# Kernel tuning notes

Hardware: AMD Instinct MI355X
Metric: run time of the kernel (lower is better)

## Reference

```python
import jax, jax.numpy as jnp
import numpy as np

N = 100000
E = 6400000
D = 512


def setup_inputs() -> dict:
    key = jax.random.key(0)
    k1, k2, k3, k4 = jax.random.split(key, 4)
    x = jax.random.normal(k1, (N, D), dtype=jnp.float32)
    edge_index = jax.random.randint(k2, (2, E), 0, N, dtype=jnp.int64)
    edge_attr = jax.random.uniform(k3, (E,), dtype=jnp.float32)
    # xavier_normal_ on (in_feat, 1) with gain=1.414: std = gain*sqrt(2/(fan_in+fan_out))
    std = 1.414 * np.sqrt(2.0 / (D + 1))
    p = jax.random.normal(k4, (D, 1), dtype=jnp.float32) * std
    b = jnp.zeros((1,), dtype=jnp.float32)
    return {"x": x, "edge_index": edge_index, "edge_attr": edge_attr, "p": p, "b": b}


def reference(x, edge_index, edge_attr, p, b):
    # Per-node gate: sigmoid(x @ p + b), shape [N]
    diag_val = jax.nn.sigmoid(jnp.matmul(x, p) + b).reshape(-1)
    # spspmm(A, diag(d)) scales each edge value by d[col] = d[edge_index[1]]
    adj_mat_val = edge_attr * diag_val[edge_index[1]]
    return edge_index, adj_mat_val
```

## Files before the change

kernel.cpp:

```cpp
#include <hip/hip_runtime.h>
#include <math.h>


__global__ __launch_bounds__(256) void gate_kernel(
    const float* __restrict__ x,
    const float* __restrict__ p,
    const float* __restrict__ b,
    float* __restrict__ gate,
    int N)
{
    const int wave_id = (blockIdx.x * blockDim.x + threadIdx.x) >> 6;
    const int lane    = threadIdx.x & 63;
    const int nwaves  = (gridDim.x * blockDim.x) >> 6;
    const float bb = b[0];

    const float4* pr = (const float4*)p;
    float4 p0 = pr[lane * 2];
    float4 p1 = pr[lane * 2 + 1];

    for (int row = wave_id; row < N; row += nwaves) {
        const float4* xr = (const float4*)(x + (size_t)row * 512);
        float4 x0 = xr[lane * 2];
        float4 x1 = xr[lane * 2 + 1];
        float s = x0.x * p0.x + x0.y * p0.y + x0.z * p0.z + x0.w * p0.w
                + x1.x * p1.x + x1.y * p1.y + x1.z * p1.z + x1.w * p1.w;
        #pragma unroll
        for (int off = 32; off > 0; off >>= 1)
            s += __shfl_down(s, off, 64);
        if (lane == 0) {
            float t = s + bb;
            gate[row] = 1.0f / (1.0f + __expf(-t));
        }
    }
}

__global__ __launch_bounds__(256) void edge_kernel(
    const int*   __restrict__ edge_index,
    const float* __restrict__ edge_attr,
    const float* __restrict__ gate,
    float* __restrict__ out,
    int E)
{
    const int tid    = blockIdx.x * blockDim.x + threadIdx.x;
    const int stride = gridDim.x * blockDim.x;

    const int EI4 = (2 * E) >> 2;
    const int EV4 = E >> 2;

    const int4*  ei4  = (const int4*)edge_index;
    float4*      out4 = (float4*)out;
    for (int i = tid; i < EI4; i += stride) {
        int4 v = ei4[i];
        out4[i] = make_float4((float)v.x, (float)v.y, (float)v.z, (float)v.w);
    }

    const int4*   col4 = (const int4*)(edge_index + E);
    const float4* ea4  = (const float4*)edge_attr;
    float4*       ov4  = (float4*)(out + 2 * (size_t)E);
    for (int i = tid; i < EV4; i += stride) {
        int4   c = col4[i];
        float4 a = ea4[i];
        float4 r;
        r.x = a.x * gate[c.x];
        r.y = a.y * gate[c.y];
        r.z = a.z * gate[c.z];
        r.w = a.w * gate[c.w];
        ov4[i] = r;
    }
}

extern "C" void kernel_launch(void* const* d_in, const int* in_sizes, int n_in,
                              void* d_out, int out_size, void* d_ws, size_t ws_size,
                              hipStream_t stream) {
    const float* x          = (const float*)d_in[0];
    const int*   edge_index = (const int*)  d_in[1];
    const float* edge_attr  = (const float*)d_in[2];
    const float* p          = (const float*)d_in[3];
    const float* b          = (const float*)d_in[4];

    const int D = in_sizes[3];
    const int N = in_sizes[0] / D;
    const int E = in_sizes[2];

    float* gate = (float*)d_ws;
    float* out  = (float*)d_out;

    int gate_blocks = (N + 3) / 4;
    gate_kernel<<<gate_blocks, 256, 0, stream>>>(x, p, b, gate, N);

    int edge_blocks = ((2 * E / 4) + 255) / 256;
    edge_kernel<<<edge_blocks, 256, 0, stream>>>(edge_index, edge_attr, gate, out, E);
}
```

Baseline: 370.2 us.

## Process two rows per wave in gate kernel and fuse edge index copy into value loop

The gate kernel now has each wave compute two rows, with a strided lane layout where lane i reads float4 i and i+64, so consecutive lanes load contiguous addresses. This gives more loads in flight per wave and uses half the waves. The edge kernel merges the index-to-float conversion loop into the value loop, so each thread reads row, col and attr once and writes all three outputs. This removes a second pass and reuses the already loaded column indices. The edge grid is halved to match.

```diff
diff --git a/kernel.cpp b/kernel.cpp
--- a/kernel.cpp
+++ b/kernel.cpp
@@ -11,25 +11,40 @@
 {
     const int wave_id = (blockIdx.x * blockDim.x + threadIdx.x) >> 6;
     const int lane    = threadIdx.x & 63;
-    const int nwaves  = (gridDim.x * blockDim.x) >> 6;
     const float bb = b[0];
 
     const float4* pr = (const float4*)p;
-    float4 p0 = pr[lane * 2];
-    float4 p1 = pr[lane * 2 + 1];
+    const float4 p0 = pr[lane];
+    const float4 p1 = pr[lane + 64];
 
-    for (int row = wave_id; row < N; row += nwaves) {
-        const float4* xr = (const float4*)(x + (size_t)row * 512);
-        float4 x0 = xr[lane * 2];
-        float4 x1 = xr[lane * 2 + 1];
-        float s = x0.x * p0.x + x0.y * p0.y + x0.z * p0.z + x0.w * p0.w
-                + x1.x * p1.x + x1.y * p1.y + x1.z * p1.z + x1.w * p1.w;
-        #pragma unroll
-        for (int off = 32; off > 0; off >>= 1)
-            s += __shfl_down(s, off, 64);
-        if (lane == 0) {
-            float t = s + bb;
-            gate[row] = 1.0f / (1.0f + __expf(-t));
+    const int row0 = wave_id * 2;
+    if (row0 >= N) return;
+    const bool two = (row0 + 1) < N;
+
+    const float4* xr0 = (const float4*)(x + (size_t)row0 * 512);
+    const float4* xr1 = (const float4*)(x + (size_t)(two ? row0 + 1 : row0) * 512);
+
+    float4 a0 = xr0[lane];
+    float4 a1 = xr0[lane + 64];
+    float4 c0 = xr1[lane];
+    float4 c1 = xr1[lane + 64];
+
+    float s0 = a0.x * p0.x + a0.y * p0.y + a0.z * p0.z + a0.w * p0.w
+             + a1.x * p1.x + a1.y * p1.y + a1.z * p1.z + a1.w * p1.w;
+    float s1 = c0.x * p0.x + c0.y * p0.y + c0.z * p0.z + c0.w * p0.w
+             + c1.x * p1.x + c1.y * p1.y + c1.z * p1.z + c1.w * p1.w;
+
+    #pragma unroll
+    for (int off = 32; off > 0; off >>= 1) {
+        s0 += __shfl_down(s0, off, 64);
+        s1 += __shfl_down(s1, off, 64);
+    }
+    if (lane == 0) {
+        float t0 = s0 + bb;
+        gate[row0] = 1.0f / (1.0f + __expf(-t0));
+        if (two) {
+            float t1 = s1 + bb;
+            gate[row0 + 1] = 1.0f / (1.0f + __expf(-t1));
         }
     }
 }
@@ -44,28 +59,30 @@
     const int tid    = blockIdx.x * blockDim.x + threadIdx.x;
     const int stride = gridDim.x * blockDim.x;
 
-    const int EI4 = (2 * E) >> 2;
     const int EV4 = E >> 2;
 
-    const int4*  ei4  = (const int4*)edge_index;
-    float4*      out4 = (float4*)out;
-    for (int i = tid; i < EI4; i += stride) {
-        int4 v = ei4[i];
-        out4[i] = make_float4((float)v.x, (float)v.y, (float)v.z, (float)v.w);
-    }
-
+    const int4*   row4 = (const int4*)edge_index;
     const int4*   col4 = (const int4*)(edge_index + E);
     const float4* ea4  = (const float4*)edge_attr;
-    float4*       ov4  = (float4*)(out + 2 * (size_t)E);
+
+    float4* outR = (float4*)out;
+    float4* outC = (float4*)(out + (size_t)E);
+    float4* outV = (float4*)(out + 2 * (size_t)E);
+
     for (int i = tid; i < EV4; i += stride) {
+        int4   r = row4[i];
         int4   c = col4[i];
         float4 a = ea4[i];
-        float4 r;
-        r.x = a.x * gate[c.x];
-        r.y = a.y * gate[c.y];
-        r.z = a.z * gate[c.z];
-        r.w = a.w * gate[c.w];
-        ov4[i] = r;
+
+        outR[i] = make_float4((float)r.x, (float)r.y, (float)r.z, (float)r.w);
+        outC[i] = make_float4((float)c.x, (float)c.y, (float)c.z, (float)c.w);
+
+        float4 v;
+        v.x = a.x * gate[c.x];
+        v.y = a.y * gate[c.y];
+        v.z = a.z * gate[c.z];
+        v.w = a.w * gate[c.w];
+        outV[i] = v;
     }
 }
 
@@ -85,9 +102,10 @@
     float* gate = (float*)d_ws;
     float* out  = (float*)d_out;
 
-    int gate_blocks = (N + 3) / 4;
+    int gate_waves  = (N + 1) / 2;
+    int gate_blocks = (gate_waves + 3) / 4;
     gate_kernel<<<gate_blocks, 256, 0, stream>>>(x, p, b, gate, N);
 
-    int edge_blocks = ((2 * E / 4) + 255) / 256;
+    int edge_blocks = ((E / 4) + 255) / 256;
     edge_kernel<<<edge_blocks, 256, 0, stream>>>(edge_index, edge_attr, gate, out, E);
 }
```

After: 363.4 us. Within noise of the previous version (-1.8%).

## Fuse edge index conversion with gated value pass and batch gate rows per wave

Applied to the files above, without the earlier changes.

The edge kernel now processes row indices, column indices and values in one pass per thread, so column indices are read once instead of twice, with two quads per thread and nontemporal loads and stores. The gate kernel assigns four rows per wave with eight independent streaming loads in flight and a single vector store of the four gates. The intent is to cut redundant memory traffic and raise memory-level parallelism. The trade-off is removing the grid-stride loops, which assumes E is a multiple of 8 and requires an aligned workspace for the vector gate store.

```diff
diff --git a/kernel.cpp b/kernel.cpp
--- a/kernel.cpp
+++ b/kernel.cpp
@@ -1,6 +1,9 @@
 #include <hip/hip_runtime.h>
 #include <math.h>
 
+
+typedef float vf4 __attribute__((ext_vector_type(4)));
+typedef int   vi4 __attribute__((ext_vector_type(4)));
 
 __global__ __launch_bounds__(256) void gate_kernel(
     const float* __restrict__ x,
@@ -11,25 +14,62 @@
 {
     const int wave_id = (blockIdx.x * blockDim.x + threadIdx.x) >> 6;
     const int lane    = threadIdx.x & 63;
-    const int nwaves  = (gridDim.x * blockDim.x) >> 6;
     const float bb = b[0];
 
-    const float4* pr = (const float4*)p;
-    float4 p0 = pr[lane * 2];
-    float4 p1 = pr[lane * 2 + 1];
+    const vf4* pr = (const vf4*)p;
+    const vf4 p0 = pr[lane];
+    const vf4 p1 = pr[lane + 64];
 
-    for (int row = wave_id; row < N; row += nwaves) {
-        const float4* xr = (const float4*)(x + (size_t)row * 512);
-        float4 x0 = xr[lane * 2];
-        float4 x1 = xr[lane * 2 + 1];
-        float s = x0.x * p0.x + x0.y * p0.y + x0.z * p0.z + x0.w * p0.w
-                + x1.x * p1.x + x1.y * p1.y + x1.z * p1.z + x1.w * p1.w;
+    const int row0 = wave_id * 4;
+    if (row0 >= N) return;
+
+    if (row0 + 3 < N) {
+        const vf4* xr = (const vf4*)(x + (size_t)row0 * 512);
+        vf4 a0 = __builtin_nontemporal_load(xr + lane);
+        vf4 a1 = __builtin_nontemporal_load(xr + lane + 64);
+        vf4 b0 = __builtin_nontemporal_load(xr + lane + 128);
+        vf4 b1 = __builtin_nontemporal_load(xr + lane + 192);
+        vf4 c0 = __builtin_nontemporal_load(xr + lane + 256);
+        vf4 c1 = __builtin_nontemporal_load(xr + lane + 320);
+        vf4 d0 = __builtin_nontemporal_load(xr + lane + 384);
+        vf4 d1 = __builtin_nontemporal_load(xr + lane + 448);
+
+        float s0 = a0.x * p0.x + a0.y * p0.y + a0.z * p0.z + a0.w * p0.w
+                 + a1.x * p1.x + a1.y * p1.y + a1.z * p1.z + a1.w * p1.w;
+        float s1 = b0.x * p0.x + b0.y * p0.y + b0.z * p0.z + b0.w * p0.w
+                 + b1.x * p1.x + b1.y * p1.y + b1.z * p1.z + b1.w * p1.w;
+        float s2 = c0.x * p0.x + c0.y * p0.y + c0.z * p0.z + c0.w * p0.w
+                 + c1.x * p1.x + c1.y * p1.y + c1.z * p1.z + c1.w * p1.w;
+        float s3 = d0.x * p0.x + d0.y * p0.y + d0.z * p0.z + d0.w * p0.w
+                 + d1.x * p1.x + d1.y * p1.y + d1.z * p1.z + d1.w * p1.w;
+
         #pragma unroll
-        for (int off = 32; off > 0; off >>= 1)
-            s += __shfl_down(s, off, 64);
+        for (int off = 32; off > 0; off >>= 1) {
+            s0 += __shfl_down(s0, off, 64);
+            s1 += __shfl_down(s1, off, 64);
+            s2 += __shfl_down(s2, off, 64);
+            s3 += __shfl_down(s3, off, 64);
+        }
         if (lane == 0) {
-            float t = s + bb;
-            gate[row] = 1.0f / (1.0f + __expf(-t));
+            vf4 g;
+            g.x = 1.0f / (1.0f + __expf(-(s0 + bb)));
+            g.y = 1.0f / (1.0f + __expf(-(s1 + bb)));
+            g.z = 1.0f / (1.0f + __expf(-(s2 + bb)));
+            g.w = 1.0f / (1.0f + __expf(-(s3 + bb)));
+            *(vf4*)(gate + row0) = g;
+        }
+    } else {
+        for (int row = row0; row < N; ++row) {
+            const vf4* xr = (const vf4*)(x + (size_t)row * 512);
+            vf4 x0 = xr[lane];
+            vf4 x1 = xr[lane + 64];
+            float s = x0.x * p0.x + x0.y * p0.y + x0.z * p0.z + x0.w * p0.w
+                    + x1.x * p1.x + x1.y * p1.y + x1.z * p1.z + x1.w * p1.w;
+            #pragma unroll
+            for (int off = 32; off > 0; off >>= 1)
+                s += __shfl_down(s, off, 64);
+            if (lane == 0)
+                gate[row] = 1.0f / (1.0f + __expf(-(s + bb)));
         }
     }
 }
@@ -41,32 +81,44 @@
     float* __restrict__ out,
     int E)
 {
-    const int tid    = blockIdx.x * blockDim.x + threadIdx.x;
-    const int stride = gridDim.x * blockDim.x;
+    const int tid = blockIdx.x * blockDim.x + threadIdx.x;
+    const int EV4 = E >> 2;
+    const int q0  = tid * 2;
+    if (q0 >= EV4) return;
 
-    const int EI4 = (2 * E) >> 2;
-    const int EV4 = E >> 2;
+    const vi4* row4 = (const vi4*)edge_index;
+    const vi4* col4 = (const vi4*)(edge_index + E);
+    const vf4* ea4  = (const vf4*)edge_attr;
 
-    const int4*  ei4  = (const int4*)edge_index;
-    float4*      out4 = (float4*)out;
-    for (int i = tid; i < EI4; i += stride) {
-        int4 v = ei4[i];
-        out4[i] = make_float4((float)v.x, (float)v.y, (float)v.z, (float)v.w);
-    }
+    vf4* outR = (vf4*)out;
+    vf4* outC = (vf4*)(out + (size_t)E);
+    vf4* outV = (vf4*)(out + 2 * (size_t)E);
 
-    const int4*   col4 = (const int4*)(edge_index + E);
-    const float4* ea4  = (const float4*)edge_attr;
-    float4*       ov4  = (float4*)(out + 2 * (size_t)E);
-    for (int i = tid; i < EV4; i += stride) {
-        int4   c = col4[i];
-        float4 a = ea4[i];
-        float4 r;
-        r.x = a.x * gate[c.x];
-        r.y = a.y * gate[c.y];
-        r.z = a.z * gate[c.z];
-        r.w = a.w * gate[c.w];
-        ov4[i] = r;
-    }
+    vi4 c0 = __builtin_nontemporal_load(col4 + q0);
+    vi4 c1 = __builtin_nontemporal_load(col4 + q0 + 1);
+    vi4 r0 = __builtin_nontemporal_load(row4 + q0);
+    vi4 r1 = __builtin_nontemporal_load(row4 + q0 + 1);
+    vf4 a0 = __builtin_nontemporal_load(ea4 + q0);
+    vf4 a1 = __builtin_nontemporal_load(ea4 + q0 + 1);
+
+    float g0x = gate[c0.x], g0y = gate[c0.y], g0z = gate[c0.z], g0w = gate[c0.w];
+    float g1x = gate[c1.x], g1y = gate[c1.y], g1z = gate[c1.z], g1w = gate[c1.w];
+
+    vf4 fr0; fr0.x = (float)r0.x; fr0.y = (float)r0.y; fr0.z = (float)r0.z; fr0.w = (float)r0.w;
+    vf4 fr1; fr1.x = (float)r1.x; fr1.y = (float)r1.y; fr1.z = (float)r1.z; fr1.w = (float)r1.w;
+    vf4 fc0; fc0.x = (float)c0.x; fc0.y = (float)c0.y; fc0.z = (float)c0.z; fc0.w = (float)c0.w;
+    vf4 fc1; fc1.x = (float)c1.x; fc1.y = (float)c1.y; fc1.z = (float)c1.z; fc1.w = (float)c1.w;
+
+    __builtin_nontemporal_store(fr0, outR + q0);
+    __builtin_nontemporal_store(fr1, outR + q0 + 1);
+    __builtin_nontemporal_store(fc0, outC + q0);
+    __builtin_nontemporal_store(fc1, outC + q0 + 1);
+
+    vf4 v0, v1;
+    v0.x = a0.x * g0x;  v0.y = a0.y * g0y;  v0.z = a0.z * g0z;  v0.w = a0.w * g0w;
+    v1.x = a1.x * g1x;  v1.y = a1.y * g1y;  v1.z = a1.z * g1z;  v1.w = a1.w * g1w;
+    __builtin_nontemporal_store(v0, outV + q0);
+    __builtin_nontemporal_store(v1, outV + q0 + 1);
 }
 
 extern "C" void kernel_launch(void* const* d_in, const int* in_sizes, int n_in,
@@ -85,9 +137,11 @@
     float* gate = (float*)d_ws;
     float* out  = (float*)d_out;
 
-    int gate_blocks = (N + 3) / 4;
+    int gate_waves  = (N + 3) / 4;
+    int gate_blocks = (gate_waves + 3) / 4;
     gate_kernel<<<gate_blocks, 256, 0, stream>>>(x, p, b, gate, N);
 
-    int edge_blocks = ((2 * E / 4) + 255) / 256;
+    int edge_threads = (E >> 2) / 2;
+    int edge_blocks  = (edge_threads + 255) / 256;
     edge_kernel<<<edge_blocks, 256, 0, stream>>>(edge_index, edge_attr, gate, out, E);
 }
```

New measurement: 351.3 us, median of 2. -5.1%, faster.
